# Kernel tuning notes

Hardware: AMD Instinct MI355X
Metric: run time of the kernel (lower is better)

Reference implementation:

```python
import jax, jax.numpy as jnp
import numpy as np

# SMPL kinematic tree: parent joint index for each of the 24 joints (root = -1 -> stored as 0, unused)
SMPL_PARENTS = np.array([0, 0, 0, 0, 1, 2, 3, 4, 5, 6, 7, 8, 9, 9, 9, 12, 13, 14, 16, 17, 18, 19, 20, 21], dtype=np.int32)

V = 6890  # vertices
J = 24    # joints
B = 1024  # batch


def setup_inputs() -> dict:
    key = jax.random.key(0)
    ks = jax.random.split(key, 8)
    return {
        "shape_params": jax.random.normal(ks[0], (B, 10), dtype=jnp.float32),
        "pose_params": jax.random.normal(ks[1], (B, 72), dtype=jnp.float32) * 0.3,
        "v_template": jax.random.normal(ks[2], (V, 3), dtype=jnp.float32),
        "shapedirs": jax.random.normal(ks[3], (10, V * 3), dtype=jnp.float32) * 0.01,
        "J_regressor": jax.random.uniform(ks[4], (V, J), dtype=jnp.float32) / V,
        "posedirs": jax.random.normal(ks[5], (207, V * 3), dtype=jnp.float32) * 0.01,
        "weights": jax.nn.softmax(jax.random.normal(ks[6], (V, J), dtype=jnp.float32), axis=-1),
        "joint_regressor": jax.random.uniform(ks[7], (V, 19), dtype=jnp.float32) / V,
        "parents": jnp.asarray(SMPL_PARENTS),
    }


def batch_rodrigues(pose):  # pose: [N, 3] axis-angle -> [N, 3, 3]
    angle = jnp.linalg.norm(pose + 1e-8, axis=1, keepdims=True)  # [N,1]
    r = pose / angle                                            # [N,3]
    cos = jnp.cos(angle)[:, :, None]                            # [N,1,1]
    sin = jnp.sin(angle)[:, :, None]
    outer = r[:, :, None] * r[:, None, :]                       # [N,3,3]
    z = jnp.zeros_like(r[:, 0])
    skew = jnp.stack([z, -r[:, 2], r[:, 1],
                      r[:, 2], z, -r[:, 0],
                      -r[:, 1], r[:, 0], z], axis=1).reshape(-1, 3, 3)
    eye = jnp.eye(3, dtype=pose.dtype)
    return cos * eye + (1.0 - cos) * outer + sin * skew


def make_homo(Rm, t):  # Rm: [B,3,3], t: [B,3] -> [B,4,4]
    b = Rm.shape[0]
    top = jnp.concatenate([Rm, t[:, :, None]], axis=2)          # [B,3,4]
    bottom = jnp.broadcast_to(jnp.array([0.0, 0.0, 0.0, 1.0], dtype=Rm.dtype), (b, 1, 4))
    return jnp.concatenate([top, bottom], axis=1)


def batch_rigid_transformation(Rs, Js, parents):
    # Rs: [B,24,3,3], Js: [B,24,3]
    parents = np.asarray(parents)
    results = [make_homo(Rs[:, 0], Js[:, 0])]
    for i in range(1, parents.shape[0]):
        p = int(parents[i])
        j_here = Js[:, i] - Js[:, p]
        A_here = make_homo(Rs[:, i], j_here)
        results.append(jnp.matmul(results[p], A_here))
    results = jnp.stack(results, axis=1)                        # [B,24,4,4]
    new_J = results[:, :, :3, 3]
    Js_w0 = jnp.concatenate([Js, jnp.zeros_like(Js[:, :, :1])], axis=2)  # [B,24,4]
    init_bone = jnp.einsum('bjxy,bjy->bjx', results, Js_w0)      # [B,24,4]
    # pad: place init_bone into the last column of a 4x4 (zeros elsewhere)
    init_bone = jnp.concatenate([jnp.zeros(results.shape[:3] + (3,), results.dtype),
                                 init_bone[..., None]], axis=3)  # [B,24,4,4]
    A = results - init_bone
    return new_J, A


def reference(shape_params, pose_params, v_template, shapedirs, J_regressor,
              posedirs, weights, joint_regressor, parents):
    b = shape_params.shape[0]
    # shape blend shapes
    v_shaped = (shape_params @ shapedirs).reshape(b, V, 3) + v_template  # [B,V,3]
    # joint locations from shaped mesh
    Jloc = jnp.einsum('bvc,vj->bjc', v_shaped, J_regressor)              # [B,24,3]
    # per-joint rotations
    Rs = batch_rodrigues(pose_params.reshape(-1, 3)).reshape(b, J, 3, 3)
    # pose blend shapes
    pose_feature = (Rs[:, 1:] - jnp.eye(3, dtype=Rs.dtype)).reshape(b, 207)
    v_posed = (pose_feature @ posedirs).reshape(b, V, 3) + v_shaped       # [B,V,3]
    # kinematic chain
    J_transformed, A = batch_rigid_transformation(Rs, Jloc, parents)
    # linear blend skinning
    T = jnp.einsum('vj,bjk->bvk', weights, A.reshape(b, J, 16)).reshape(b, V, 4, 4)
    v_posed_h = jnp.concatenate([v_posed, jnp.ones((b, V, 1), v_posed.dtype)], axis=2)
    verts = jnp.einsum('bvxy,bvy->bvx', T, v_posed_h)[:, :, :3]           # [B,V,3]
    joints = jnp.einsum('bvc,vj->bjc', verts, joint_regressor)            # [B,19,3]
    return verts, joints, J_transformed
```

## Files before the change

### kernel.cpp

```cpp
#include <hip/hip_runtime.h>
#include <hip/hip_bf16.h>
#include <math.h>

static constexpr int BATCH = 1024;
static constexpr int NV = 6890;
static constexpr int NJ = 24;
static constexpr int NP = 207;
static constexpr int NR = 19;
static constexpr int V3 = NV * 3;
static constexpr int KK = 7;
static constexpr int BTILES = BATCH / 16;
static constexpr int XBLK = 108;
static constexpr int NT_PAD = XBLK * 12;
static constexpr int TSTR = 196;

typedef __attribute__((ext_vector_type(8))) short bf16x8;
typedef __attribute__((ext_vector_type(4))) float f32x4;

__device__ __forceinline__ short f2bf(float x) {
  __hip_bfloat16 h = __float2bfloat16(x);
  return __builtin_bit_cast(short, h);
}

__global__ void k0_precompute(const float* __restrict__ sdirs,
                              const float* __restrict__ vtem,
                              const float* __restrict__ jreg,
                              float* __restrict__ SDJ,
                              float* __restrict__ VTJ) {
  const int jc = blockIdx.x;
  const int j = jc / 3, c = jc % 3;
  float acc[11];
#pragma unroll
  for (int k = 0; k < 11; ++k) acc[k] = 0.f;
  for (int v = threadIdx.x; v < NV; v += 256) {
    const float w = jreg[v * NJ + j];
    acc[10] += vtem[v * 3 + c] * w;
#pragma unroll
    for (int k = 0; k < 10; ++k) acc[k] += sdirs[(size_t)k * V3 + v * 3 + c] * w;
  }
  __shared__ float red[4][11];
  const int lane = threadIdx.x & 63, wv = threadIdx.x >> 6;
#pragma unroll
  for (int k = 0; k < 11; ++k) {
    float x = acc[k];
#pragma unroll
    for (int off = 32; off >= 1; off >>= 1) x += __shfl_down(x, off);
    if (lane == 0) red[wv][k] = x;
  }
  __syncthreads();
  if (threadIdx.x == 0) {
#pragma unroll
    for (int k = 0; k < 11; ++k) {
      const float s = red[0][k] + red[1][k] + red[2][k] + red[3][k];
      if (k < 10) SDJ[k * 72 + jc] = s;
      else        VTJ[jc] = s;
    }
  }
}

__global__ void k1_chain(const float* __restrict__ shape,
                         const float* __restrict__ pose,
                         const int* __restrict__ parents,
                         const float* __restrict__ SDJ,
                         const float* __restrict__ VTJ,
                         short* __restrict__ Ap,
                         float* __restrict__ Aws,
                         float* __restrict__ out_jt)
{
  const int b = blockIdx.x;
  const int t = threadIdx.x;
  const int bt = b >> 4, b16 = b & 15;
  __shared__ float sh[10];
  __shared__ float Jl[NJ][3];
  __shared__ float Rm[NJ][9];
  __shared__ float G[NJ][12];
  if (t < 10) sh[t] = shape[b * 10 + t];
  __syncthreads();
  if (t < 72) {
    float s = VTJ[t];
#pragma unroll
    for (int k = 0; k < 10; ++k) s += sh[k] * SDJ[k * 72 + t];
    Jl[t / 3][t % 3] = s;
  }
  if (t < NJ) {
    const float px = pose[b * 72 + t * 3 + 0];
    const float py = pose[b * 72 + t * 3 + 1];
    const float pz = pose[b * 72 + t * 3 + 2];
    const float ax = px + 1e-8f, ay = py + 1e-8f, az = pz + 1e-8f;
    const float ang = sqrtf(ax * ax + ay * ay + az * az);
    const float inv = 1.f / ang;
    const float rx = px * inv, ry = py * inv, rz = pz * inv;
    const float cc = cosf(ang), ss = sinf(ang), mc = 1.f - cc;
    float R[9];
    R[0] = cc + mc * rx * rx;      R[1] = mc * rx * ry - ss * rz;  R[2] = mc * rx * rz + ss * ry;
    R[3] = mc * rx * ry + ss * rz; R[4] = cc + mc * ry * ry;       R[5] = mc * ry * rz - ss * rx;
    R[6] = mc * rx * rz - ss * ry; R[7] = mc * ry * rz + ss * rx;  R[8] = cc + mc * rz * rz;
#pragma unroll
    for (int i = 0; i < 9; ++i) Rm[t][i] = R[i];
    if (t >= 1) {
#pragma unroll
      for (int i = 0; i < 9; ++i) {
        const float val = R[i] - ((i == 0 || i == 4 || i == 8) ? 1.f : 0.f);
        const int k = (t - 1) * 9 + i;
        const int kk = k >> 5, g = (k & 31) >> 3, jj = k & 7;
        Ap[(((size_t)bt * KK + kk) * 64 + b16 + 16 * g) * 8 + jj] = f2bf(val);
      }
    }
  }
  if (t >= 24 && t < 41) {
    const int k = t + 183;
    const int kk = k >> 5, g = (k & 31) >> 3, jj = k & 7;
    Ap[(((size_t)bt * KK + kk) * 64 + b16 + 16 * g) * 8 + jj] = 0;
  }
  __syncthreads();
  if (t == 0) {
#pragma unroll
    for (int r = 0; r < 3; ++r) {
      G[0][r * 4 + 0] = Rm[0][r * 3 + 0];
      G[0][r * 4 + 1] = Rm[0][r * 3 + 1];
      G[0][r * 4 + 2] = Rm[0][r * 3 + 2];
      G[0][r * 4 + 3] = Jl[0][r];
    }
    for (int i = 1; i < NJ; ++i) {
      const int p = parents[i];
      const float tx = Jl[i][0] - Jl[p][0];
      const float ty = Jl[i][1] - Jl[p][1];
      const float tz = Jl[i][2] - Jl[p][2];
#pragma unroll
      for (int r = 0; r < 3; ++r) {
        const float a0 = G[p][r * 4 + 0], a1 = G[p][r * 4 + 1], a2 = G[p][r * 4 + 2];
        G[i][r * 4 + 0] = a0 * Rm[i][0] + a1 * Rm[i][3] + a2 * Rm[i][6];
        G[i][r * 4 + 1] = a0 * Rm[i][1] + a1 * Rm[i][4] + a2 * Rm[i][7];
        G[i][r * 4 + 2] = a0 * Rm[i][2] + a1 * Rm[i][5] + a2 * Rm[i][8];
        G[i][r * 4 + 3] = a0 * tx + a1 * ty + a2 * tz + G[p][r * 4 + 3];
      }
    }
  }
  __syncthreads();
  if (t < NJ) {
    const float jx = Jl[t][0], jy = Jl[t][1], jz = Jl[t][2];
    float* Ab = Aws + (size_t)b * (NJ * 12) + t * 12;
#pragma unroll
    for (int r = 0; r < 3; ++r) {
      const float g0 = G[t][r * 4 + 0], g1 = G[t][r * 4 + 1];
      const float g2 = G[t][r * 4 + 2], g3 = G[t][r * 4 + 3];
      Ab[r * 4 + 0] = g0; Ab[r * 4 + 1] = g1; Ab[r * 4 + 2] = g2;
      Ab[r * 4 + 3] = g3 - (g0 * jx + g1 * jy + g2 * jz);
      out_jt[(size_t)b * (NJ * 3) + t * 3 + r] = g3;
    }
  }
}

__global__ void k_packB(const float* __restrict__ pdirs, short* __restrict__ Bp) {
  const int blk = blockIdx.x;
  const int nt = blk / KK, kk = blk % KK;
  const int lane = threadIdx.x;
  const int n = nt * 16 + (lane & 15);
  const int k0 = kk * 32 + (lane >> 4) * 8;
  short o[8];
#pragma unroll
  for (int j = 0; j < 8; ++j) {
    const int k = k0 + j;
    o[j] = f2bf((k < NP && n < V3) ? pdirs[(size_t)k * V3 + n] : 0.f);
  }
  *(bf16x8*)(Bp + ((size_t)blk * 64 + lane) * 8) = *(const bf16x8*)o;
}

__global__ void __launch_bounds__(256) k2_fused(
    const short* __restrict__ Ap, const short* __restrict__ Bp,
    const float* __restrict__ Aws, const float* __restrict__ shape,
    const float* __restrict__ vtem, const float* __restrict__ sdirs,
    const float* __restrict__ wgt, float* __restrict__ verts) {
  __shared__ float Cls[16 * TSTR];
  __shared__ float Alds[16 * NJ * 12];
  const int w = threadIdx.x >> 6, lane = threadIdx.x & 63;
  const int g = lane >> 4, c = lane & 15;
  const int x = blockIdx.x, bt = blockIdx.y;
  const int b0 = bt * 16;

  for (int i = threadIdx.x; i < 16 * NJ * 12; i += 256)
    Alds[i] = Aws[(size_t)b0 * (NJ * 12) + i];

  {
    const bf16x8* Av = (const bf16x8*)Ap;
    const bf16x8* Bv = (const bf16x8*)Bp;
    bf16x8 a[KK];
#pragma unroll
    for (int kk = 0; kk < KK; ++kk) a[kk] = Av[(size_t)(bt * KK + kk) * 64 + lane];
#pragma unroll
    for (int s = 0; s < 3; ++s) {
      const int nt_g = x * 12 + w * 3 + s;
      f32x4 acc = {0.f, 0.f, 0.f, 0.f};
#pragma unroll
      for (int kk = 0; kk < KK; ++kk) {
        const bf16x8 bfrag = Bv[(size_t)(nt_g * KK + kk) * 64 + lane];
        acc = __builtin_amdgcn_mfma_f32_16x16x32_bf16(a[kk], bfrag, acc, 0, 0, 0);
      }
#pragma unroll
      for (int r = 0; r < 4; ++r)
        Cls[(4 * g + r) * TSTR + (w * 3 + s) * 16 + c] = acc[r];
    }
  }
  __syncthreads();

  const int v = x * 64 + lane;
  const int vv = v < NV ? v : (NV - 1);
  float vph[4][3];
  {
    const float t0 = vtem[vv * 3 + 0], t1 = vtem[vv * 3 + 1], t2 = vtem[vv * 3 + 2];
#pragma unroll
    for (int i = 0; i < 4; ++i) {
      const int bl = w + 4 * i;
      vph[i][0] = Cls[bl * TSTR + lane * 3 + 0] + t0;
      vph[i][1] = Cls[bl * TSTR + lane * 3 + 1] + t1;
      vph[i][2] = Cls[bl * TSTR + lane * 3 + 2] + t2;
    }
  }
#pragma unroll
  for (int k = 0; k < 10; ++k) {
    const float d0 = sdirs[(size_t)k * V3 + vv * 3 + 0];
    const float d1 = sdirs[(size_t)k * V3 + vv * 3 + 1];
    const float d2 = sdirs[(size_t)k * V3 + vv * 3 + 2];
#pragma unroll
    for (int i = 0; i < 4; ++i) {
      const float s = shape[(b0 + w + 4 * i) * 10 + k];
      vph[i][0] += s * d0; vph[i][1] += s * d1; vph[i][2] += s * d2;
    }
  }

  float wj[NJ];
#pragma unroll
  for (int j = 0; j < NJ; ++j) wj[j] = wgt[vv * NJ + j];

  float T[4][12];
#pragma unroll
  for (int i = 0; i < 4; ++i)
#pragma unroll
    for (int k = 0; k < 12; ++k) T[i][k] = 0.f;

#pragma unroll
  for (int j = 0; j < NJ; ++j) {
    const float wv_ = wj[j];
#pragma unroll
    for (int i = 0; i < 4; ++i) {
      const int bl = w + 4 * i;
      const f32x4 a0 = *(const f32x4*)&Alds[bl * (NJ * 12) + j * 12 + 0];
      const f32x4 a1 = *(const f32x4*)&Alds[bl * (NJ * 12) + j * 12 + 4];
      const f32x4 a2 = *(const f32x4*)&Alds[bl * (NJ * 12) + j * 12 + 8];
#pragma unroll
      for (int k = 0; k < 4; ++k) {
        T[i][k + 0] += wv_ * a0[k];
        T[i][k + 4] += wv_ * a1[k];
        T[i][k + 8] += wv_ * a2[k];
      }
    }
  }
  if (v < NV) {
#pragma unroll
    for (int i = 0; i < 4; ++i) {
      const int bl = w + 4 * i;
      const float X = vph[i][0], Y = vph[i][1], Z = vph[i][2];
      const size_t o = (size_t)(b0 + bl) * V3 + (size_t)v * 3;
      verts[o + 0] = T[i][0] * X + T[i][1] * Y + T[i][2]  * Z + T[i][3];
      verts[o + 1] = T[i][4] * X + T[i][5] * Y + T[i][6]  * Z + T[i][7];
      verts[o + 2] = T[i][8] * X + T[i][9] * Y + T[i][10] * Z + T[i][11];
    }
  }
}

__global__ void k3_joints(const float* __restrict__ verts,
                          const float* __restrict__ jr2,
                          float* __restrict__ out_joints) {
  const int b = blockIdx.x;
  float a[NR * 3];
#pragma unroll
  for (int q = 0; q < NR * 3; ++q) a[q] = 0.f;
  for (int v = threadIdx.x; v < NV; v += 256) {
    const size_t o = (size_t)b * V3 + (size_t)v * 3;
    const float x = verts[o + 0];
    const float y = verts[o + 1];
    const float z = verts[o + 2];
#pragma unroll
    for (int r = 0; r < NR; ++r) {
      const float w = jr2[v * NR + r];
      a[r * 3 + 0] += w * x; a[r * 3 + 1] += w * y; a[r * 3 + 2] += w * z;
    }
  }
  __shared__ float red[4][NR * 3];
  const int lane = threadIdx.x & 63, wv = threadIdx.x >> 6;
#pragma unroll
  for (int q = 0; q < NR * 3; ++q) {
    float x = a[q];
#pragma unroll
    for (int off = 32; off >= 1; off >>= 1) x += __shfl_down(x, off);
    if (lane == 0) red[wv][q] = x;
  }
  __syncthreads();
  if (threadIdx.x < NR * 3) {
    const float s = red[0][threadIdx.x] + red[1][threadIdx.x] +
                    red[2][threadIdx.x] + red[3][threadIdx.x];
    out_joints[(size_t)b * (NR * 3) + threadIdx.x] = s;
  }
}

extern "C" void kernel_launch(void* const* d_in, const int* in_sizes, int n_in,
                              void* d_out, int out_size, void* d_ws, size_t ws_size,
                              hipStream_t stream) {
  const float* shape = (const float*)d_in[0];
  const float* pose  = (const float*)d_in[1];
  const float* vtem  = (const float*)d_in[2];
  const float* sdirs = (const float*)d_in[3];
  const float* jreg  = (const float*)d_in[4];
  const float* pdirs = (const float*)d_in[5];
  const float* wgt   = (const float*)d_in[6];
  const float* jr2   = (const float*)d_in[7];
  const int*   par   = (const int*)d_in[8];

  float* ws  = (float*)d_ws;
  float* SDJ = ws;
  float* VTJ = ws + 720;
  float* Aws = ws + 1024;
  short* Ap  = (short*)(Aws + BATCH * NJ * 12);
  short* Bp  = Ap + (size_t)BTILES * KK * 64 * 8;

  float* out        = (float*)d_out;
  float* out_verts  = out;
  float* out_joints = out + (size_t)BATCH * NV * 3;
  float* out_jt     = out_joints + (size_t)BATCH * NR * 3;

  k_packB<<<dim3(NT_PAD * KK), dim3(64), 0, stream>>>(pdirs, Bp);
  k0_precompute<<<dim3(72), dim3(256), 0, stream>>>(sdirs, vtem, jreg, SDJ, VTJ);
  k1_chain<<<dim3(BATCH), dim3(128), 0, stream>>>(shape, pose, par, SDJ, VTJ, Ap, Aws, out_jt);
  k2_fused<<<dim3(XBLK, BTILES), dim3(256), 0, stream>>>(
      Ap, Bp, Aws, shape, vtem, sdirs, wgt, out_verts);
  k3_joints<<<dim3(BATCH), dim3(256), 0, stream>>>(out_verts, jr2, out_joints);
}
```

Measured before the change: 229.5 us.

## Loop batch tiles inside fused skinning kernel and process two batches per joints block

The fused GEMM+skinning kernel now runs a grid of 108x8 blocks, and each block loops over 8 batch tiles. The posedirs B-fragments, vertex template and skinning weights are loaded into registers once per block and reused across those tiles instead of being reloaded for every tile. The joints kernel now handles two batch rows per block so each joint-regressor weight load serves both. The cost is much higher register pressure from holding 21 bf16x8 fragments plus 24 weights, which may lower occupancy, and fewer blocks (864) to hide latency.

```diff
diff --git a/kernel.cpp b/kernel.cpp
--- a/kernel.cpp
+++ b/kernel.cpp
@@ -13,6 +13,8 @@
 static constexpr int XBLK = 108;
 static constexpr int NT_PAD = XBLK * 12;
 static constexpr int TSTR = 196;
+static constexpr int GRIDY = 8;
+static constexpr int NBT = BTILES / GRIDY;
 
 typedef __attribute__((ext_vector_type(8))) short bf16x8;
 typedef __attribute__((ext_vector_type(4))) float f32x4;
@@ -175,39 +177,52 @@
   __shared__ float Alds[16 * NJ * 12];
   const int w = threadIdx.x >> 6, lane = threadIdx.x & 63;
   const int g = lane >> 4, c = lane & 15;
-  const int x = blockIdx.x, bt = blockIdx.y;
-  const int b0 = bt * 16;
-
-  for (int i = threadIdx.x; i < 16 * NJ * 12; i += 256)
-    Alds[i] = Aws[(size_t)b0 * (NJ * 12) + i];
-
-  {
-    const bf16x8* Av = (const bf16x8*)Ap;
-    const bf16x8* Bv = (const bf16x8*)Bp;
-    bf16x8 a[KK];
-#pragma unroll
-    for (int kk = 0; kk < KK; ++kk) a[kk] = Av[(size_t)(bt * KK + kk) * 64 + lane];
-#pragma unroll
-    for (int s = 0; s < 3; ++s) {
-      const int nt_g = x * 12 + w * 3 + s;
-      f32x4 acc = {0.f, 0.f, 0.f, 0.f};
-#pragma unroll
-      for (int kk = 0; kk < KK; ++kk) {
-        const bf16x8 bfrag = Bv[(size_t)(nt_g * KK + kk) * 64 + lane];
-        acc = __builtin_amdgcn_mfma_f32_16x16x32_bf16(a[kk], bfrag, acc, 0, 0, 0);
-      }
-#pragma unroll
-      for (int r = 0; r < 4; ++r)
-        Cls[(4 * g + r) * TSTR + (w * 3 + s) * 16 + c] = acc[r];
-    }
-  }
-  __syncthreads();
+  const int x = blockIdx.x;
+  const int bt0 = blockIdx.y * NBT;
+  const bf16x8* Av = (const bf16x8*)Ap;
+  const bf16x8* Bv = (const bf16x8*)Bp;
 
   const int v = x * 64 + lane;
   const int vv = v < NV ? v : (NV - 1);
-  float vph[4][3];
-  {
-    const float t0 = vtem[vv * 3 + 0], t1 = vtem[vv * 3 + 1], t2 = vtem[vv * 3 + 2];
+  const float t0 = vtem[vv * 3 + 0], t1 = vtem[vv * 3 + 1], t2 = vtem[vv * 3 + 2];
+  float wj[NJ];
+#pragma unroll
+  for (int j = 0; j < NJ; ++j) wj[j] = wgt[vv * NJ + j];
+
+  bf16x8 bfr[3][KK];
+#pragma unroll
+  for (int s = 0; s < 3; ++s) {
+    const int nt_g = x * 12 + w * 3 + s;
+#pragma unroll
+    for (int kk = 0; kk < KK; ++kk)
+      bfr[s][kk] = Bv[(size_t)(nt_g * KK + kk) * 64 + lane];
+  }
+
+  for (int bt = bt0; bt < bt0 + NBT; ++bt) {
+    const int b0 = bt * 16;
+    __syncthreads();
+
+    for (int i = threadIdx.x; i < 16 * NJ * 12; i += 256)
+      Alds[i] = Aws[(size_t)b0 * (NJ * 12) + i];
+
+    {
+      bf16x8 a[KK];
+#pragma unroll
+      for (int kk = 0; kk < KK; ++kk) a[kk] = Av[(size_t)(bt * KK + kk) * 64 + lane];
+#pragma unroll
+      for (int s = 0; s < 3; ++s) {
+        f32x4 acc = {0.f, 0.f, 0.f, 0.f};
+#pragma unroll
+        for (int kk = 0; kk < KK; ++kk)
+          acc = __builtin_amdgcn_mfma_f32_16x16x32_bf16(a[kk], bfr[s][kk], acc, 0, 0, 0);
+#pragma unroll
+        for (int r = 0; r < 4; ++r)
+          Cls[(4 * g + r) * TSTR + (w * 3 + s) * 16 + c] = acc[r];
+      }
+    }
+    __syncthreads();
+
+    float vph[4][3];
 #pragma unroll
     for (int i = 0; i < 4; ++i) {
       const int bl = w + 4 * i;
@@ -215,55 +230,52 @@
       vph[i][1] = Cls[bl * TSTR + lane * 3 + 1] + t1;
       vph[i][2] = Cls[bl * TSTR + lane * 3 + 2] + t2;
     }
-  }
-#pragma unroll
-  for (int k = 0; k < 10; ++k) {
-    const float d0 = sdirs[(size_t)k * V3 + vv * 3 + 0];
-    const float d1 = sdirs[(size_t)k * V3 + vv * 3 + 1];
-    const float d2 = sdirs[(size_t)k * V3 + vv * 3 + 2];
-#pragma unroll
-    for (int i = 0; i < 4; ++i) {
-      const float s = shape[(b0 + w + 4 * i) * 10 + k];
-      vph[i][0] += s * d0; vph[i][1] += s * d1; vph[i][2] += s * d2;
-    }
-  }
-
-  float wj[NJ];
-#pragma unroll
-  for (int j = 0; j < NJ; ++j) wj[j] = wgt[vv * NJ + j];
-
-  float T[4][12];
-#pragma unroll
-  for (int i = 0; i < 4; ++i)
-#pragma unroll
-    for (int k = 0; k < 12; ++k) T[i][k] = 0.f;
-
-#pragma unroll
-  for (int j = 0; j < NJ; ++j) {
-    const float wv_ = wj[j];
-#pragma unroll
-    for (int i = 0; i < 4; ++i) {
-      const int bl = w + 4 * i;
-      const f32x4 a0 = *(const f32x4*)&Alds[bl * (NJ * 12) + j * 12 + 0];
-      const f32x4 a1 = *(const f32x4*)&Alds[bl * (NJ * 12) + j * 12 + 4];
-      const f32x4 a2 = *(const f32x4*)&Alds[bl * (NJ * 12) + j * 12 + 8];
-#pragma unroll
-      for (int k = 0; k < 4; ++k) {
-        T[i][k + 0] += wv_ * a0[k];
-        T[i][k + 4] += wv_ * a1[k];
-        T[i][k + 8] += wv_ * a2[k];
-      }
-    }
-  }
-  if (v < NV) {
-#pragma unroll
-    for (int i = 0; i < 4; ++i) {
-      const int bl = w + 4 * i;
-      const float X = vph[i][0], Y = vph[i][1], Z = vph[i][2];
-      const size_t o = (size_t)(b0 + bl) * V3 + (size_t)v * 3;
-      verts[o + 0] = T[i][0] * X + T[i][1] * Y + T[i][2]  * Z + T[i][3];
-      verts[o + 1] = T[i][4] * X + T[i][5] * Y + T[i][6]  * Z + T[i][7];
-      verts[o + 2] = T[i][8] * X + T[i][9] * Y + T[i][10] * Z + T[i][11];
+#pragma unroll
+    for (int k = 0; k < 10; ++k) {
+      const float d0 = sdirs[(size_t)k * V3 + vv * 3 + 0];
+      const float d1 = sdirs[(size_t)k * V3 + vv * 3 + 1];
+      const float d2 = sdirs[(size_t)k * V3 + vv * 3 + 2];
+#pragma unroll
+      for (int i = 0; i < 4; ++i) {
+        const float s = shape[(b0 + w + 4 * i) * 10 + k];
+        vph[i][0] += s * d0; vph[i][1] += s * d1; vph[i][2] += s * d2;
+      }
+    }
+
+    float T[4][12];
+#pragma unroll
+    for (int i = 0; i < 4; ++i)
+#pragma unroll
+      for (int k = 0; k < 12; ++k) T[i][k] = 0.f;
+
+#pragma unroll
+    for (int j = 0; j < NJ; ++j) {
+      const float wv_ = wj[j];
+#pragma unroll
+      for (int i = 0; i < 4; ++i) {
+        const int bl = w + 4 * i;
+        const f32x4 a0 = *(const f32x4*)&Alds[bl * (NJ * 12) + j * 12 + 0];
+        const f32x4 a1 = *(const f32x4*)&Alds[bl * (NJ * 12) + j * 12 + 4];
+        const f32x4 a2 = *(const f32x4*)&Alds[bl * (NJ * 12) + j * 12 + 8];
+#pragma unroll
+        for (int k = 0; k < 4; ++k) {
+          T[i][k + 0] += wv_ * a0[k];
+          T[i][k + 4] += wv_ * a1[k];
+          T[i][k + 8] += wv_ * a2[k];
+        }
+      }
+    }
+
+    if (v < NV) {
+#pragma unroll
+      for (int i = 0; i < 4; ++i) {
+        const int bl = w + 4 * i;
+        const float X = vph[i][0], Y = vph[i][1], Z = vph[i][2];
+        const size_t o = (size_t)(b0 + bl) * V3 + (size_t)v * 3;
+        verts[o + 0] = T[i][0] * X + T[i][1] * Y + T[i][2]  * Z + T[i][3];
+        verts[o + 1] = T[i][4] * X + T[i][5] * Y + T[i][6]  * Z + T[i][7];
+        verts[o + 2] = T[i][8] * X + T[i][9] * Y + T[i][10] * Z + T[i][11];
+      }
     }
   }
 }
@@ -271,35 +283,47 @@
 __global__ void k3_joints(const float* __restrict__ verts,
                           const float* __restrict__ jr2,
                           float* __restrict__ out_joints) {
-  const int b = blockIdx.x;
-  float a[NR * 3];
-#pragma unroll
-  for (int q = 0; q < NR * 3; ++q) a[q] = 0.f;
+  const int b0 = blockIdx.x * 2;
+  float a[2][NR * 3];
+#pragma unroll
+  for (int bb = 0; bb < 2; ++bb)
+#pragma unroll
+    for (int q = 0; q < NR * 3; ++q) a[bb][q] = 0.f;
   for (int v = threadIdx.x; v < NV; v += 256) {
-    const size_t o = (size_t)b * V3 + (size_t)v * 3;
-    const float x = verts[o + 0];
-    const float y = verts[o + 1];
-    const float z = verts[o + 2];
-#pragma unroll
-    for (int r = 0; r < NR; ++r) {
-      const float w = jr2[v * NR + r];
-      a[r * 3 + 0] += w * x; a[r * 3 + 1] += w * y; a[r * 3 + 2] += w * z;
-    }
-  }
-  __shared__ float red[4][NR * 3];
+    float wr[NR];
+#pragma unroll
+    for (int r = 0; r < NR; ++r) wr[r] = jr2[v * NR + r];
+#pragma unroll
+    for (int bb = 0; bb < 2; ++bb) {
+      const size_t o = (size_t)(b0 + bb) * V3 + (size_t)v * 3;
+      const float x = verts[o + 0];
+      const float y = verts[o + 1];
+      const float z = verts[o + 2];
+#pragma unroll
+      for (int r = 0; r < NR; ++r) {
+        a[bb][r * 3 + 0] += wr[r] * x;
+        a[bb][r * 3 + 1] += wr[r] * y;
+        a[bb][r * 3 + 2] += wr[r] * z;
+      }
+    }
+  }
+  __shared__ float red[4][2 * NR * 3];
   const int lane = threadIdx.x & 63, wv = threadIdx.x >> 6;
 #pragma unroll
-  for (int q = 0; q < NR * 3; ++q) {
-    float x = a[q];
-#pragma unroll
-    for (int off = 32; off >= 1; off >>= 1) x += __shfl_down(x, off);
-    if (lane == 0) red[wv][q] = x;
-  }
-  __syncthreads();
-  if (threadIdx.x < NR * 3) {
-    const float s = red[0][threadIdx.x] + red[1][threadIdx.x] +
-                    red[2][threadIdx.x] + red[3][threadIdx.x];
-    out_joints[(size_t)b * (NR * 3) + threadIdx.x] = s;
+  for (int bb = 0; bb < 2; ++bb)
+#pragma unroll
+    for (int q = 0; q < NR * 3; ++q) {
+      float x = a[bb][q];
+#pragma unroll
+      for (int off = 32; off >= 1; off >>= 1) x += __shfl_down(x, off);
+      if (lane == 0) red[wv][bb * NR * 3 + q] = x;
+    }
+  __syncthreads();
+  if (threadIdx.x < 2 * NR * 3) {
+    const int t = threadIdx.x;
+    const int bb = t / (NR * 3), qq = t % (NR * 3);
+    const float s = red[0][t] + red[1][t] + red[2][t] + red[3][t];
+    out_joints[(size_t)(b0 + bb) * (NR * 3) + qq] = s;
   }
 }
 
@@ -331,7 +355,7 @@
   k_packB<<<dim3(NT_PAD * KK), dim3(64), 0, stream>>>(pdirs, Bp);
   k0_precompute<<<dim3(72), dim3(256), 0, stream>>>(sdirs, vtem, jreg, SDJ, VTJ);
   k1_chain<<<dim3(BATCH), dim3(128), 0, stream>>>(shape, pose, par, SDJ, VTJ, Ap, Aws, out_jt);
-  k2_fused<<<dim3(XBLK, BTILES), dim3(256), 0, stream>>>(
+  k2_fused<<<dim3(XBLK, GRIDY), dim3(256), 0, stream>>>(
       Ap, Bp, Aws, shape, vtem, sdirs, wgt, out_verts);
-  k3_joints<<<dim3(BATCH), dim3(256), 0, stream>>>(out_verts, jr2, out_joints);
-}
+  k3_joints<<<dim3(BATCH / 2), dim3(256), 0, stream>>>(out_verts, jr2, out_joints);
+}
```

Result: slower. 696.3 us (+203.4%).
